# Optimization experiments

Hardware: AMD Instinct MI355X
Metric: run time of the kernel (lower is better)

The kernel has to match this reference:

```python
import jax, jax.numpy as jnp
import numpy as np

N, M = 120000, 32
VX, VY = 0.16, 0.16
X_OFF = VX / 2 + 0.0          # vx/2 + pc_range[0]
Y_OFF = VY / 2 + (-39.68)     # vy/2 + pc_range[1]
BN_EPS = 1e-3


def setup_inputs() -> dict:
    key = jax.random.key(0)
    k1, k2, k3, k4, k5 = jax.random.split(key, 5)
    features = jax.random.normal(k1, (N, M, 4), dtype=jnp.float32)
    num_points = jax.random.randint(k2, (N,), 1, M + 1)              # >=1 point per pillar
    cy = jax.random.randint(k3, (N, 1), 0, 496)
    cx = jax.random.randint(k4, (N, 1), 0, 432)
    zeros = jnp.zeros((N, 2), dtype=jnp.int32)
    coors = jnp.concatenate([zeros, cy, cx], axis=1)                 # (N,4): [b, z, y, x]
    W = jax.random.normal(k5, (63, 9), dtype=jnp.float32) * 0.1      # Linear(9->63), no bias
    gamma = jnp.ones((63,), jnp.float32)
    beta = jnp.zeros((63,), jnp.float32)
    running_mean = jnp.zeros((63,), jnp.float32)
    running_var = jnp.ones((63,), jnp.float32)
    return {"features": features, "num_points": num_points, "coors": coors,
            "W": W, "gamma": gamma, "beta": beta,
            "running_mean": running_mean, "running_var": running_var}


def reference(features, num_points, coors, W, gamma, beta, running_mean, running_var):
    dt = features.dtype
    npf = num_points.astype(dt)[:, None, None]                        # (N,1,1)
    # distance to pillar centroid (xyz mean over points)
    voxels_mean = features[:, :, :3].sum(axis=1, keepdims=True) / npf
    centroid_dist = features[:, :, :3] - voxels_mean                  # (N,M,3)
    # offset from pillar base center (detached in the original)
    fxy = jax.lax.stop_gradient(features[:, :, :2])
    cx = fxy[:, :, 0] - (coors[:, 3].astype(dt)[:, None] * VX + X_OFF)
    cy = fxy[:, :, 1] - (coors[:, 2].astype(dt)[:, None] * VY + Y_OFF)
    base_center = jnp.stack([cx, cy], axis=-1)                        # (N,M,2)
    feats = jnp.concatenate([features, centroid_dist, base_center], axis=-1)  # (N,M,9)
    # zero out padded points
    mask = (jnp.arange(feats.shape[1])[None, :] < num_points[:, None]).astype(dt)[:, :, None]
    feats = feats * mask
    # PFNLayer (last layer, mode='max'): linear -> BN (eval stats) -> relu -> max over points
    x = jnp.einsum('nmc,uc->nmu', feats, W)                           # (N,M,63)
    inv = gamma / jnp.sqrt(running_var + BN_EPS)
    x = x * inv + (beta - running_mean * inv)
    x = jax.nn.relu(x)
    x_max = x.max(axis=1)                                             # (N,63)
    return jnp.concatenate([x_max, num_points.astype(dt)[:, None]], axis=-1)  # (N,64)
```

## Files before the change

kernel.cpp:

```cpp
#include <hip/hip_runtime.h>
#include <hip/hip_bf16.h>

typedef unsigned int u32;
typedef unsigned short u16;
typedef __attribute__((ext_vector_type(8))) short bf16x8;
typedef __attribute__((ext_vector_type(16))) float f32x16;
typedef __attribute__((ext_vector_type(4))) u32 u32x4;


#define XOFF (0.08f)
#define YOFF (0.08f - 39.68f)

__device__ __forceinline__ u32 f2bf_bits(float f) {
    union { float f; u32 u; } v; v.f = f;
    u32 u = v.u;
    u += 0x7fffu + ((u >> 16) & 1u);
    return u >> 16;
}
__device__ __forceinline__ short bf1(float f) { return (short)f2bf_bits(f); }

__device__ __forceinline__ u32 pk2(float lo, float hi) {
    __hip_bfloat162 h = __float22bfloat162_rn(make_float2(lo, hi));
    union { __hip_bfloat162 h; u32 u; } v; v.h = h;
    return v.u;
}

__device__ __forceinline__ float vmax16(const f32x16 v) {
    float a = fmaxf(fmaxf(v[0], v[1]), fmaxf(v[2], v[3]));
    float b = fmaxf(fmaxf(v[4], v[5]), fmaxf(v[6], v[7]));
    float c = fmaxf(fmaxf(v[8], v[9]), fmaxf(v[10], v[11]));
    float d = fmaxf(fmaxf(v[12], v[13]), fmaxf(v[14], v[15]));
    return fmaxf(fmaxf(a, b), fmaxf(c, d));
}

__global__ __launch_bounds__(256, 4)
void pfn_mfma(const float* __restrict__ features,
              const int* __restrict__ num_points,
              const int* __restrict__ coors,
              const float* __restrict__ W,
              const float* __restrict__ gamma,
              const float* __restrict__ beta,
              const float* __restrict__ rmean,
              const float* __restrict__ rvar,
              float* __restrict__ out,
              int n_total)
{
    const int lane = threadIdx.x & 63;
    const int wid  = threadIdx.x >> 6;
    const int half = lane >> 5;
    const int m    = lane & 31;
    const int waves_total = gridDim.x * 4;
    const int gwave = blockIdx.x * 4 + wid;

    const int c0 = m, c1 = 32 + m;
    const float inv0   = gamma[c0] / sqrtf(rvar[c0] + 1e-3f);
    const float shift0 = beta[c0] - rmean[c0] * inv0;
    float inv1 = 0.0f, shift1 = 0.0f;
    if (c1 < 63) {
        inv1   = gamma[c1] / sqrtf(rvar[c1] + 1e-3f);
        shift1 = beta[c1] - rmean[c1] * inv1;
    }
    const float shift_me = half ? shift1 : shift0;

    bf16x8 b0, b1;
#pragma unroll
    for (int j = 0; j < 8; ++j) {
        const int k = half * 8 + j;
        b0[j] = bf1((k < 9) ? W[c0 * 9 + k] * inv0 : 0.0f);
        b1[j] = bf1((k < 9 && c1 < 63) ? W[c1 * 9 + k] * inv1 : 0.0f);
    }

    const float4* featv = reinterpret_cast<const float4*>(features);
    const int iters = (n_total + 2 * waves_total - 1) / (2 * waves_total);

    float4 q = make_float4(0.f, 0.f, 0.f, 0.f);
    int   npts = 1;
    float cxo = 0.f, cyo = 0.f;
    {
        const int n_h = gwave * 2 + half;
        if (n_h < n_total) {
            npts = num_points[n_h];
            cxo = (float)coors[n_h * 4 + 3] * 0.16f + XOFF;
            cyo = (float)coors[n_h * 4 + 2] * 0.16f + YOFF;
            q = featv[(size_t)n_h * 32 + m];
        }
    }

    for (int it = 0; it < iters; ++it) {
        const int nA = (gwave + it * waves_total) * 2;

        float4 qn = make_float4(0.f, 0.f, 0.f, 0.f);
        int   npn = 1;
        float cxn = 0.f, cyn = 0.f;
        if (it + 1 < iters) {
            const int n_h = (gwave + (it + 1) * waves_total) * 2 + half;
            if (n_h < n_total) {
                npn = num_points[n_h];
                cxn = (float)coors[n_h * 4 + 3] * 0.16f + XOFF;
                cyn = (float)coors[n_h * 4 + 2] * 0.16f + YOFF;
                qn = featv[(size_t)n_h * 32 + m];
            }
        }

        float sx = q.x, sy = q.y, sz = q.z;
#pragma unroll
        for (int d = 1; d < 32; d <<= 1) {
            sx += __shfl_xor(sx, d, 32);
            sy += __shfl_xor(sy, d, 32);
            sz += __shfl_xor(sz, d, 32);
        }
        const float rnp = 1.0f / (float)npts;
        const float mx = sx * rnp, my = sy * rnp, mz = sz * rnp;

        u32 p0 = pk2(q.x, q.y);
        u32 p1 = pk2(q.z, q.w);
        u32 p2 = pk2(q.x - mx, q.y - my);
        u32 p3 = pk2(q.z - mz, q.x - cxo);
        u32 p4 = pk2(q.y - cyo, 0.0f);
        if (m >= npts) { p0 = 0; p1 = 0; p2 = 0; p3 = 0; p4 = 0; }

        const u32 x0 = __shfl_xor(p0, 32);
        const u32 x1 = __shfl_xor(p1, 32);
        const u32 x2 = __shfl_xor(p2, 32);
        const u32 x3 = __shfl_xor(p3, 32);
        const u32 x4 = __shfl_xor(p4, 32);

        u32x4 adw, bdw;
        adw[0] = half ? x4 : p0;  adw[1] = half ? 0u : p1;
        adw[2] = half ? 0u : p2;  adw[3] = half ? 0u : p3;
        bdw[0] = half ? p4 : x0;  bdw[1] = half ? 0u : x1;
        bdw[2] = half ? 0u : x2;  bdw[3] = half ? 0u : x3;
        const bf16x8 aA = __builtin_bit_cast(bf16x8, adw);
        const bf16x8 aB = __builtin_bit_cast(bf16x8, bdw);

        f32x16 cA0 = {}, cA1 = {}, cB0 = {}, cB1 = {};
        cA0 = __builtin_amdgcn_mfma_f32_32x32x16_bf16(aA, b0, cA0, 0, 0, 0);
        cA1 = __builtin_amdgcn_mfma_f32_32x32x16_bf16(aA, b1, cA1, 0, 0, 0);
        cB0 = __builtin_amdgcn_mfma_f32_32x32x16_bf16(aB, b0, cB0, 0, 0, 0);
        cB1 = __builtin_amdgcn_mfma_f32_32x32x16_bf16(aB, b1, cB1, 0, 0, 0);

        float tA0 = vmax16(cA0), tA1 = vmax16(cA1);
        float tB0 = vmax16(cB0), tB1 = vmax16(cB1);
        tA0 = fmaxf(tA0, __shfl_xor(tA0, 32));
        tA1 = fmaxf(tA1, __shfl_xor(tA1, 32));
        tB0 = fmaxf(tB0, __shfl_xor(tB0, 32));
        tB1 = fmaxf(tB1, __shfl_xor(tB1, 32));

        float vA = fmaxf((half ? tA1 : tA0) + shift_me, 0.0f);
        float vB = fmaxf((half ? tB1 : tB0) + shift_me, 0.0f);

        const float npf = (float)npts;
        const float npA = __shfl(npf, 0);
        const float npB = __shfl(npf, 32);
        if (lane == 63) { vA = npA; vB = npB; }

        if (nA < n_total)     out[(size_t)nA * 64 + lane] = vA;
        if (nA + 1 < n_total) out[(size_t)(nA + 1) * 64 + lane] = vB;

        q = qn; npts = npn; cxo = cxn; cyo = cyn;
    }
}

extern "C" void kernel_launch(void* const* d_in, const int* in_sizes, int n_in,
                              void* d_out, int out_size, void* d_ws, size_t ws_size,
                              hipStream_t stream) {
    const float* features   = (const float*)d_in[0];
    const int*   num_points = (const int*)d_in[1];
    const int*   coors      = (const int*)d_in[2];
    const float* W          = (const float*)d_in[3];
    const float* gamma      = (const float*)d_in[4];
    const float* beta       = (const float*)d_in[5];
    const float* rmean      = (const float*)d_in[6];
    const float* rvar       = (const float*)d_in[7];
    float* out              = (float*)d_out;

    const int n_total = in_sizes[1];

    const int blocks = 1024;
    pfn_mfma<<<blocks, 256, 0, stream>>>(features, num_points, coors, W,
                                         gamma, beta, rmean, rvar, out, n_total);
}
```

Before: 132.8 us.

## Replace software-prefetched persistent loop with large grid and higher occupancy

Drops the register-held software prefetch of the next pillar pair and the fixed 1024-block persistent grid. Instead it launches enough blocks that each wave handles about two pillar pairs and raises the launch-bounds occupancy hint to 8 blocks per CU, relying on the hardware to hide memory latency across waves. It also loads the two coordinate ints as one int2 and uses 32-bit index math. The risk is losing explicit load/compute overlap inside each wave, and paying more per-wave setup for the BN/weight fragments since waves run far fewer iterations.

```diff
diff --git a/kernel.cpp b/kernel.cpp
--- a/kernel.cpp
+++ b/kernel.cpp
@@ -2,7 +2,6 @@
 #include <hip/hip_bf16.h>
 
 typedef unsigned int u32;
-typedef unsigned short u16;
 typedef __attribute__((ext_vector_type(8))) short bf16x8;
 typedef __attribute__((ext_vector_type(16))) float f32x16;
 typedef __attribute__((ext_vector_type(4))) u32 u32x4;
@@ -33,7 +32,7 @@
     return fmaxf(fmaxf(a, b), fmaxf(c, d));
 }
 
-__global__ __launch_bounds__(256, 4)
+__global__ __launch_bounds__(256, 8)
 void pfn_mfma(const float* __restrict__ features,
               const int* __restrict__ num_points,
               const int* __restrict__ coors,
@@ -71,35 +70,22 @@
     }
 
     const float4* featv = reinterpret_cast<const float4*>(features);
-    const int iters = (n_total + 2 * waves_total - 1) / (2 * waves_total);
+    const int n_pairs = (n_total + 1) >> 1;
 
-    float4 q = make_float4(0.f, 0.f, 0.f, 0.f);
-    int   npts = 1;
-    float cxo = 0.f, cyo = 0.f;
-    {
-        const int n_h = gwave * 2 + half;
-        if (n_h < n_total) {
+    for (int pair = gwave; pair < n_pairs; pair += waves_total) {
+        const int nA  = pair * 2;
+        const int n_h = nA + half;
+        const bool act = (n_h < n_total);
+
+        int npts = 1;
+        float cxo = 0.f, cyo = 0.f;
+        float4 q = make_float4(0.f, 0.f, 0.f, 0.f);
+        if (act) {
             npts = num_points[n_h];
-            cxo = (float)coors[n_h * 4 + 3] * 0.16f + XOFF;
-            cyo = (float)coors[n_h * 4 + 2] * 0.16f + YOFF;
-            q = featv[(size_t)n_h * 32 + m];
-        }
-    }
-
-    for (int it = 0; it < iters; ++it) {
-        const int nA = (gwave + it * waves_total) * 2;
-
-        float4 qn = make_float4(0.f, 0.f, 0.f, 0.f);
-        int   npn = 1;
-        float cxn = 0.f, cyn = 0.f;
-        if (it + 1 < iters) {
-            const int n_h = (gwave + (it + 1) * waves_total) * 2 + half;
-            if (n_h < n_total) {
-                npn = num_points[n_h];
-                cxn = (float)coors[n_h * 4 + 3] * 0.16f + XOFF;
-                cyn = (float)coors[n_h * 4 + 2] * 0.16f + YOFF;
-                qn = featv[(size_t)n_h * 32 + m];
-            }
+            const int2 cc = *reinterpret_cast<const int2*>(coors + n_h * 4 + 2);
+            cxo = (float)cc.y * 0.16f + XOFF;
+            cyo = (float)cc.x * 0.16f + YOFF;
+            q = featv[n_h * 32 + m];
         }
 
         float sx = q.x, sy = q.y, sz = q.z;
@@ -154,10 +140,8 @@
         const float npB = __shfl(npf, 32);
         if (lane == 63) { vA = npA; vB = npB; }
 
-        if (nA < n_total)     out[(size_t)nA * 64 + lane] = vA;
-        if (nA + 1 < n_total) out[(size_t)(nA + 1) * 64 + lane] = vB;
-
-        q = qn; npts = npn; cxo = cxn; cyo = cyn;
+        if (nA < n_total)     out[nA * 64 + lane] = vA;
+        if (nA + 1 < n_total) out[(nA + 1) * 64 + lane] = vB;
     }
 }
 
@@ -176,7 +160,9 @@
 
     const int n_total = in_sizes[1];
 
-    const int blocks = 1024;
+    const int n_pairs = (n_total + 1) / 2;
+    const int waves   = (n_pairs + 1) / 2;
+    const int blocks  = (waves + 3) / 4;
     pfn_mfma<<<blocks, 256, 0, stream>>>(features, num_points, coors, W,
                                          gamma, beta, rmean, rvar, out, n_total);
 }
```

Result: slower. 195.6 us (+47.3%).
